# Kernel tuning notes

Measured on AMD Instinct MI355X. Metric: run time of the kernel, lower is better.

Reference implementation:

```python
import jax, jax.numpy as jnp
import numpy as np

B, C, H, W = 4, 256, 64, 64
N = H * W


def _conv1x1(x, w, b):
    # x: [B,C,H,W], w: [O,C], b: [O]  (1x1 conv == per-pixel linear)
    return jnp.einsum('bchw,oc->bohw', x, w) + b[None, :, None, None]


def setup_inputs() -> dict:
    key = jax.random.key(0)
    ks = jax.random.split(key, 11)
    s = 1.0 / np.sqrt(C)
    x = jax.random.normal(ks[0], (B, C, H, W), dtype=jnp.float32)
    mkw = lambda k: jax.random.normal(k, (C, C), dtype=jnp.float32) * s
    mkb = lambda k: jax.random.normal(k, (C,), dtype=jnp.float32) * 0.01
    return {
        'x': x,
        'w_teta': mkw(ks[1]), 'b_teta': mkb(ks[2]),
        'w_fi': mkw(ks[3]), 'b_fi': mkb(ks[4]),
        'w_gi': mkw(ks[5]), 'b_gi': mkb(ks[6]),
        'w_o1': mkw(ks[7]), 'b_o1': mkb(ks[8]),
        'w_o2': mkw(ks[9]), 'b_o2': mkb(ks[10]),
    }


def reference(x, w_teta, b_teta, w_fi, b_fi, w_gi, b_gi, w_o1, b_o1, w_o2, b_o2):
    b, c, h, w = x.shape
    n = h * w
    # 1x1 projections, flattened to [B,C,N]
    x1 = _conv1x1(x, w_teta, b_teta).reshape(b, c, n)
    x2 = _conv1x1(x, w_fi, b_fi).reshape(b, c, n)
    x3 = _conv1x1(x, w_gi, b_gi).reshape(b, c, n)
    # NOTE: original uses .view (memory reinterpretation), NOT transpose
    x1 = x1.reshape(b, n, c)
    x3 = x3.reshape(b, n, c)
    scores = jnp.einsum('bnc,bcm->bnm', x1, x2)      # [B,N,N]
    s_row = jax.nn.softmax(scores, axis=2)
    s_col = jax.nn.softmax(scores, axis=1)
    y1 = jnp.einsum('bnm,bmc->bnc', s_row, x3)       # [B,N,C]
    y2 = jnp.einsum('bnm,bmc->bnc', s_col, x3)
    # transpose(1,2) then view -> contiguous transpose + reshape
    y1 = jnp.swapaxes(y1, 1, 2).reshape(b, c, h, w)
    y2 = jnp.swapaxes(y2, 1, 2).reshape(b, c, h, w)
    o1 = _conv1x1(y1, w_o1, b_o1)
    o2 = _conv1x1(y2, w_o2, b_o2)
    xx = jnp.concatenate([x, x], axis=1)             # [B,2C,H,W]
    agg = jnp.concatenate([o1, o2], axis=1)
    return jax.nn.relu(xx + agg)
```

## Files before the change

kernel.cpp:

```cpp
#include <hip/hip_runtime.h>

#define BB   4
#define CC   256
#define NPIX 4096
#define AST2 40
#define YST  72

typedef __attribute__((ext_vector_type(8)))  short bf16x8;
typedef __attribute__((ext_vector_type(8)))  _Float16 f16x8;
typedef __attribute__((ext_vector_type(4)))  short short4v;
typedef __attribute__((ext_vector_type(16))) float f32x16;

__device__ __forceinline__ short f2h(float f) {
    _Float16 h = (_Float16)f;
    return __builtin_bit_cast(short, h);
}
__device__ __forceinline__ int cdrow(int r, int l5) {
    return (r & 3) + 8 * (r >> 2) + 4 * l5;
}
__device__ __forceinline__ short s_enc(float v) {
    float c = fmaxf(fminf(v, 127.9f), -127.9f);
    return (short)__float2int_rn(c * 256.0f);
}
__device__ __forceinline__ float s_dec(short v) {
    return (float)v * (1.0f / 256.0f);
}

__device__ __forceinline__ void mfma_core_f16(
    const short* __restrict__ A, const short* __restrict__ B, f32x16 acc[2][2])
{
    __shared__ short LA[128 * AST2], LB[128 * AST2];
    const int t = threadIdx.x;
    const int lane = t & 63, w = t >> 6;
    const int l31 = lane & 31, l5 = lane >> 5;
    const int nq = (w & 1) * 64, mq = (w >> 1) * 64;
    const int sr = t >> 1;
    const int sk = (t & 1) * 16;
    const size_t gs = (size_t)sr * 256 + sk;
    const int ls = sr * AST2 + sk;

    bf16x8 rA0 = *(const bf16x8*)(A + gs);
    bf16x8 rA1 = *(const bf16x8*)(A + gs + 8);
    bf16x8 rB0 = *(const bf16x8*)(B + gs);
    bf16x8 rB1 = *(const bf16x8*)(B + gs + 8);

    for (int k0 = 0; k0 < 256; k0 += 32) {
        __syncthreads();
        *(bf16x8*)&LA[ls]     = rA0;
        *(bf16x8*)&LA[ls + 8] = rA1;
        *(bf16x8*)&LB[ls]     = rB0;
        *(bf16x8*)&LB[ls + 8] = rB1;
        __syncthreads();
        if (k0 + 32 < 256) {
            size_t g = gs + k0 + 32;
            rA0 = *(const bf16x8*)(A + g);
            rA1 = *(const bf16x8*)(A + g + 8);
            rB0 = *(const bf16x8*)(B + g);
            rB1 = *(const bf16x8*)(B + g + 8);
        }
#pragma unroll
        for (int ks = 0; ks < 2; ks++) {
            f16x8 a[2], b[2];
#pragma unroll
            for (int s = 0; s < 2; s++) {
                a[s] = *(const f16x8*)&LA[(nq + s * 32 + l31) * AST2 + ks * 16 + l5 * 8];
                b[s] = *(const f16x8*)&LB[(mq + s * 32 + l31) * AST2 + ks * 16 + l5 * 8];
            }
#pragma unroll
            for (int s = 0; s < 2; s++)
#pragma unroll
                for (int u = 0; u < 2; u++)
                    acc[s][u] = __builtin_amdgcn_mfma_f32_32x32x16_f16(a[s], b[u], acc[s][u], 0, 0, 0);
        }
    }
}


__global__ __launch_bounds__(256) void pack_w5(
    const float* __restrict__ w0, const float* __restrict__ w1,
    const float* __restrict__ w2, const float* __restrict__ w3,
    const float* __restrict__ w4, short* __restrict__ wall)
{
    int which = blockIdx.y;
    const float* w = which == 0 ? w0 : which == 1 ? w1 : which == 2 ? w2
                   : which == 3 ? w3 : w4;
    int idx = blockIdx.x * 1024 + threadIdx.x * 4;
    float4 v = *(const float4*)(w + idx);
    short4v h;
    h.x = f2h(v.x); h.y = f2h(v.y); h.z = f2h(v.z); h.w = f2h(v.w);
    *(short4v*)(wall + which * 65536 + idx) = h;
}

__global__ __launch_bounds__(256) void pack_t_f16(
    const float* __restrict__ in, short* __restrict__ o16)
{
    __shared__ short T[32][36];
    const int b  = blockIdx.z;
    const int n0 = blockIdx.x * 32;
    const int c0 = blockIdx.y * 32;
    const float* src = in + (size_t)b * CC * NPIX;
    const int t = threadIdx.x;
    const int r = t >> 3, q = t & 7;
    float4 v = *(const float4*)(src + (size_t)(c0 + r) * NPIX + n0 + q * 4);
    T[q * 4 + 0][r] = f2h(v.x);
    T[q * 4 + 1][r] = f2h(v.y);
    T[q * 4 + 2][r] = f2h(v.z);
    T[q * 4 + 3][r] = f2h(v.w);
    __syncthreads();
    short4v o;
    o.x = T[r][q * 4 + 0];
    o.y = T[r][q * 4 + 1];
    o.z = T[r][q * 4 + 2];
    o.w = T[r][q * 4 + 3];
    size_t oo = (size_t)b * CC * NPIX + (size_t)(n0 + r) * 256 + c0 + q * 4;
    *(short4v*)(o16 + oo) = o;
}

__global__ __launch_bounds__(256) void tr16_cn(
    const short* __restrict__ in, short* __restrict__ outp)
{
    __shared__ short T[32][33];
    const int b  = blockIdx.z;
    const int n0 = blockIdx.x * 32;
    const int c0 = blockIdx.y * 32;
    const short* src = in + (size_t)b * CC * NPIX;
    short* dst = outp + (size_t)b * CC * NPIX;
    const int t = threadIdx.x;
    const int r = t >> 3, q = t & 7;
    short4v v = *(const short4v*)(src + (size_t)(c0 + r) * NPIX + n0 + q * 4);
    T[q * 4 + 0][r] = v.x;
    T[q * 4 + 1][r] = v.y;
    T[q * 4 + 2][r] = v.z;
    T[q * 4 + 3][r] = v.w;
    __syncthreads();
    short4v o;
    o.x = T[r][q * 4 + 0];
    o.y = T[r][q * 4 + 1];
    o.z = T[r][q * 4 + 2];
    o.w = T[r][q * 4 + 3];
    *(short4v*)(dst + (size_t)(n0 + r) * 256 + c0 + q * 4) = o;
}

__global__ __launch_bounds__(256) void packVt_bf(
    const short* __restrict__ x3f, short* __restrict__ Vt)
{
    __shared__ short T[32][33];
    const int b  = blockIdx.z;
    const int m0 = blockIdx.x * 32;
    const int c0 = blockIdx.y * 32;
    const short* in = x3f + (size_t)b * CC * NPIX;
    short* out = Vt + (size_t)b * CC * NPIX;
    const int t = threadIdx.x;
    const int r = t >> 3, q = t & 7;
    short4v v = *(const short4v*)(in + (size_t)(m0 + r) * CC + c0 + q * 4);
    T[q * 4 + 0][r] = v.x;
    T[q * 4 + 1][r] = v.y;
    T[q * 4 + 2][r] = v.z;
    T[q * 4 + 3][r] = v.w;
    __syncthreads();
    short4v o;
    o.x = T[r][q * 4 + 0];
    o.y = T[r][q * 4 + 1];
    o.z = T[r][q * 4 + 2];
    o.w = T[r][q * 4 + 3];
    *(short4v*)(out + (size_t)(c0 + r) * NPIX + m0 + q * 4) = o;
}


__global__ __launch_bounds__(256) void proj_mfma(
    const short* __restrict__ wpf, const short* __restrict__ xtf,
    const float* __restrict__ b_teta, const float* __restrict__ b_fi,
    const float* __restrict__ b_gi,
    short* __restrict__ x1f, short* __restrict__ x2f, short* __restrict__ x3f)
{
    const int z = blockIdx.z, p = z >> 2, b = z & 3;
    const int n0 = blockIdx.x * 128, c0 = blockIdx.y * 128;
    const size_t CN = (size_t)CC * NPIX;
    const short* Ah = wpf + p * 65536 + c0 * 256;
    const short* Bh = xtf + (size_t)b * CN + (size_t)n0 * 256;
    const float* bias = p == 0 ? b_teta : p == 1 ? b_fi : b_gi;
    short* dst = p == 0 ? x1f : p == 1 ? x2f : x3f;

    f32x16 acc[2][2] = {};
    mfma_core_f16(Ah, Bh, acc);

    const int t = threadIdx.x, lane = t & 63, w = t >> 6;
    const int l31 = lane & 31, l5 = lane >> 5;
    const int aq = (w & 1) * 64, bq = (w >> 1) * 64;
#pragma unroll
    for (int s = 0; s < 2; s++)
#pragma unroll
        for (int u = 0; u < 2; u++)
#pragma unroll
            for (int r = 0; r < 16; r++) {
                int c = c0 + aq + s * 32 + cdrow(r, l5);
                int n = n0 + bq + u * 32 + l31;
                float v = acc[s][u][r] + bias[c];
                size_t o = (size_t)b * CN + (size_t)c * NPIX + n;
                dst[o] = f2h(v);
            }
}

__global__ __launch_bounds__(256) void scores_mfma(
    const short* __restrict__ x1f, const short* __restrict__ x2tf,
    short* __restrict__ S16, float* __restrict__ pm, float* __restrict__ pl)
{
    const int m0 = blockIdx.x * 128, n0 = blockIdx.y * 128;
    f32x16 acc[2][2] = {};
    mfma_core_f16(x1f + (size_t)n0 * 256, x2tf + (size_t)m0 * 256, acc);

    const int t = threadIdx.x, lane = t & 63, w = t >> 6;
    const int l31 = lane & 31, l5 = lane >> 5;
    const int aq = (w & 1) * 64, bq = (w >> 1) * 64;
#pragma unroll
    for (int s = 0; s < 2; s++)
#pragma unroll
        for (int u = 0; u < 2; u++)
#pragma unroll
            for (int r = 0; r < 16; r++) {
                int n = n0 + aq + s * 32 + cdrow(r, l5);
                int m = m0 + bq + u * 32 + l31;
                S16[(size_t)n * NPIX + m] = s_enc(acc[s][u][r]);
            }

    const int member = w & 1;
#pragma unroll
    for (int u = 0; u < 2; u++) {
        float vmax = -1e30f;
#pragma unroll
        for (int s = 0; s < 2; s++)
#pragma unroll
            for (int r = 0; r < 16; r++) vmax = fmaxf(vmax, acc[s][u][r]);
        float vsum = 0.0f;
#pragma unroll
        for (int s = 0; s < 2; s++)
#pragma unroll
            for (int r = 0; r < 16; r++) vsum += __expf(acc[s][u][r] - vmax);
        float vmax2 = __shfl_xor(vmax, 32, 64);
        float vsum2 = __shfl_xor(vsum, 32, 64);
        float mc = fmaxf(vmax, vmax2);
        float sc = vsum * __expf(vmax - mc) + vsum2 * __expf(vmax2 - mc);
        if (l5 == 0) {
            size_t pidx = (size_t)(blockIdx.y * 2 + member) * NPIX + m0 + bq + u * 32 + l31;
            pm[pidx] = mc;
            pl[pidx] = sc;
        }
    }
}

__global__ __launch_bounds__(256) void out_mfma(
    const short* __restrict__ wof,
    const float* __restrict__ b_o1, const float* __restrict__ b_o2,
    const short* __restrict__ Yp,
    const float* __restrict__ x, float* __restrict__ out, int b)
{
    __shared__ short LA[128 * AST2], LB[128 * AST2];
    const size_t CN_ = (size_t)NPIX * CC;
    const int ch0 = blockIdx.y * 128;
    const int pix0 = blockIdx.x * 128;
    const int mode = ch0 < 256 ? 0 : 1;
    const short* W = wof + mode * 65536 + (size_t)(ch0 & 255) * 256;
    const short* Yq = Yp + (size_t)mode * 4 * CN_;
    const float* bias = mode == 0 ? b_o1 : b_o2;

    const int t = threadIdx.x, lane = t & 63, w = t >> 6;
    const int l31 = lane & 31, l5 = lane >> 5;
    const int nq = (w & 1) * 64, mq = (w >> 1) * 64;
    const int sr = t >> 1;
    const int sk = (t & 1) * 16;
    const size_t gsA = (size_t)sr * 256 + sk;
    const size_t gsB = (size_t)(pix0 + sr) * 256 + sk;
    const int ls = sr * AST2 + sk;

    f32x16 acc[2][2] = {};

    bf16x8 rA0 = *(const bf16x8*)(W + gsA);
    bf16x8 rA1 = *(const bf16x8*)(W + gsA + 8);
    f16x8 rB0, rB1;
    {
        f16x8 a0 = *(const f16x8*)(Yq + gsB);
        f16x8 a1 = *(const f16x8*)(Yq + CN_ + gsB);
        f16x8 a2 = *(const f16x8*)(Yq + 2 * CN_ + gsB);
        f16x8 a3 = *(const f16x8*)(Yq + 3 * CN_ + gsB);
        rB0 = (a0 + a1) + (a2 + a3);
        f16x8 c0 = *(const f16x8*)(Yq + gsB + 8);
        f16x8 c1 = *(const f16x8*)(Yq + CN_ + gsB + 8);
        f16x8 c2 = *(const f16x8*)(Yq + 2 * CN_ + gsB + 8);
        f16x8 c3 = *(const f16x8*)(Yq + 3 * CN_ + gsB + 8);
        rB1 = (c0 + c1) + (c2 + c3);
    }

    for (int k0 = 0; k0 < 256; k0 += 32) {
        __syncthreads();
        *(bf16x8*)&LA[ls]    = rA0;
        *(bf16x8*)&LA[ls + 8] = rA1;
        *(f16x8*)&LB[ls]     = rB0;
        *(f16x8*)&LB[ls + 8] = rB1;
        __syncthreads();
        if (k0 + 32 < 256) {
            size_t gA = gsA + k0 + 32;
            size_t gB = gsB + k0 + 32;
            rA0 = *(const bf16x8*)(W + gA);
            rA1 = *(const bf16x8*)(W + gA + 8);
            f16x8 a0 = *(const f16x8*)(Yq + gB);
            f16x8 a1 = *(const f16x8*)(Yq + CN_ + gB);
            f16x8 a2 = *(const f16x8*)(Yq + 2 * CN_ + gB);
            f16x8 a3 = *(const f16x8*)(Yq + 3 * CN_ + gB);
            rB0 = (a0 + a1) + (a2 + a3);
            f16x8 c0 = *(const f16x8*)(Yq + gB + 8);
            f16x8 c1 = *(const f16x8*)(Yq + CN_ + gB + 8);
            f16x8 c2 = *(const f16x8*)(Yq + 2 * CN_ + gB + 8);
            f16x8 c3 = *(const f16x8*)(Yq + 3 * CN_ + gB + 8);
            rB1 = (c0 + c1) + (c2 + c3);
        }
#pragma unroll
        for (int ks = 0; ks < 2; ks++) {
            f16x8 a[2], bb[2];
#pragma unroll
            for (int s = 0; s < 2; s++) {
                a[s]  = *(const f16x8*)&LA[(nq + s * 32 + l31) * AST2 + ks * 16 + l5 * 8];
                bb[s] = *(const f16x8*)&LB[(mq + s * 32 + l31) * AST2 + ks * 16 + l5 * 8];
            }
#pragma unroll
            for (int s = 0; s < 2; s++)
#pragma unroll
                for (int u = 0; u < 2; u++)
                    acc[s][u] = __builtin_amdgcn_mfma_f32_32x32x16_f16(a[s], bb[u], acc[s][u], 0, 0, 0);
        }
    }

    const int aq = (w & 1) * 64, bq = (w >> 1) * 64;
#pragma unroll
    for (int s = 0; s < 2; s++)
#pragma unroll
        for (int u = 0; u < 2; u++)
#pragma unroll
            for (int r = 0; r < 16; r++) {
                int ch = ch0 + aq + s * 32 + cdrow(r, l5);
                int pix = pix0 + bq + u * 32 + l31;
                int chm = ch & 255;
                float v = acc[s][u][r] + bias[chm] +
                          x[((size_t)b * CC + chm) * NPIX + pix];
                out[((size_t)b * 2 * CC + ch) * NPIX + pix] = fmaxf(v, 0.0f);
            }
}

__global__ __launch_bounds__(256) void colstats2_kernel(
    const float* __restrict__ pm, const float* __restrict__ pl,
    float* __restrict__ cm, float* __restrict__ cli)
{
    __shared__ float sm[4][64], sl[4][64];
    const int t = threadIdx.x;
    const int cl = t & 63, ch = t >> 6;
    const int col = blockIdx.x * 64 + cl;
    float m = -1e30f, l = 0.0f;
    for (int i = ch * 16; i < ch * 16 + 16; i++) {
        float m2 = pm[(size_t)i * NPIX + col];
        float l2 = pl[(size_t)i * NPIX + col];
        float mn = fmaxf(m, m2);
        l = l * __expf(m - mn) + l2 * __expf(m2 - mn);
        m = mn;
    }
    sm[ch][cl] = m;
    sl[ch][cl] = l;
    __syncthreads();
    if (ch == 0) {
#pragma unroll
        for (int j = 1; j < 4; j++) {
            float m2 = sm[j][cl], l2 = sl[j][cl];
            float mn = fmaxf(m, m2);
            l = l * __expf(m - mn) + l2 * __expf(m2 - mn);
            m = mn;
        }
        cm[col]  = m;
        cli[col] = 1.0f / l;
    }
}

__global__ __launch_bounds__(256) void rowexpP_kernel(
    const short* __restrict__ S16,
    const float* __restrict__ colm, const float* __restrict__ colli,
    short* __restrict__ P1, short* __restrict__ P2)
{
    const int row = blockIdx.x;
    const short* sp = S16 + (size_t)row * NPIX;
    const int t = threadIdx.x;
    const int w = t >> 6, lane = t & 63;
    __shared__ float red[4];

    float s4[16];
#pragma unroll
    for (int i = 0; i < 4; i++) {
        short4v v = *(const short4v*)(sp + (i * 256 + t) * 4);
        s4[i * 4 + 0] = s_dec(v.x);
        s4[i * 4 + 1] = s_dec(v.y);
        s4[i * 4 + 2] = s_dec(v.z);
        s4[i * 4 + 3] = s_dec(v.w);
    }

    float m = -1e30f;
#pragma unroll
    for (int i = 0; i < 16; i++) m = fmaxf(m, s4[i]);
    for (int off = 32; off; off >>= 1) m = fmaxf(m, __shfl_xor(m, off, 64));
    if (lane == 0) red[w] = m;
    __syncthreads();
    m = fmaxf(fmaxf(red[0], red[1]), fmaxf(red[2], red[3]));
    __syncthreads();

    float e[16];
    float sum = 0.0f;
#pragma unroll
    for (int i = 0; i < 16; i++) {
        e[i] = __expf(s4[i] - m);
        sum += e[i];
    }
    for (int off = 32; off; off >>= 1) sum += __shfl_xor(sum, off, 64);
    if (lane == 0) red[w] = sum;
    __syncthreads();
    float rl = 1.0f / (red[0] + red[1] + red[2] + red[3]);

    short* p1 = P1 + (size_t)row * NPIX;
    short* p2 = P2 + (size_t)row * NPIX;
#pragma unroll
    for (int i = 0; i < 4; i++) {
        int idx = (i * 256 + t) * 4;
        float4 cm4 = *(const float4*)(colm + idx);
        float4 cl4 = *(const float4*)(colli + idx);
        short4v a, bvv;
        a.x = f2h(e[i * 4 + 0] * rl);
        a.y = f2h(e[i * 4 + 1] * rl);
        a.z = f2h(e[i * 4 + 2] * rl);
        a.w = f2h(e[i * 4 + 3] * rl);
        bvv.x = f2h(__expf(s4[i * 4 + 0] - cm4.x) * cl4.x);
        bvv.y = f2h(__expf(s4[i * 4 + 1] - cm4.y) * cl4.y);
        bvv.z = f2h(__expf(s4[i * 4 + 2] - cm4.z) * cl4.z);
        bvv.w = f2h(__expf(s4[i * 4 + 3] - cm4.w) * cl4.w);
        *(short4v*)(p1 + idx) = a;
        *(short4v*)(p2 + idx) = bvv;
    }
}

__global__ __launch_bounds__(256) void ygemm_kernel(
    const short* __restrict__ P1, const short* __restrict__ P2,
    const short* __restrict__ Vt, short* __restrict__ Yp)
{
    __shared__ short LA[64 * YST];
    __shared__ short LB[256 * YST];
    const int mode = blockIdx.z, kq = blockIdx.y;
    const int n0 = blockIdx.x * 64;
    const short* A = (mode ? P2 : P1) + (size_t)n0 * NPIX;
    const short* B = Vt;
    const int kbase = kq * 1024;

    const int t = threadIdx.x, lane = t & 63, w = t >> 6;
    const int l31 = lane & 31, l5 = lane >> 5;
    const int nst = (w & 1) * 32, cb = (w >> 1) * 128;
    const int ar = t >> 2;
    const int ak = (t & 3) * 16;

    bf16x8 pa[2], pb[8];
    {
        const short* ap = A + (size_t)ar * NPIX + kbase + ak;
        pa[0] = *(const bf16x8*)ap;
        pa[1] = *(const bf16x8*)(ap + 8);
#pragma unroll
        for (int i = 0; i < 4; i++) {
            const short* bp = B + (size_t)(i * 64 + ar) * NPIX + kbase + ak;
            pb[2 * i]     = *(const bf16x8*)bp;
            pb[2 * i + 1] = *(const bf16x8*)(bp + 8);
        }
    }

    f32x16 acc[4] = {};
    for (int s = 0; s < 16; s++) {
        __syncthreads();
        *(bf16x8*)&LA[ar * YST + ak]     = pa[0];
        *(bf16x8*)&LA[ar * YST + ak + 8] = pa[1];
#pragma unroll
        for (int i = 0; i < 4; i++) {
            *(bf16x8*)&LB[(i * 64 + ar) * YST + ak]     = pb[2 * i];
            *(bf16x8*)&LB[(i * 64 + ar) * YST + ak + 8] = pb[2 * i + 1];
        }
        __syncthreads();
        if (s + 1 < 16) {
            int kg = kbase + (s + 1) * 64 + ak;
            const short* ap = A + (size_t)ar * NPIX + kg;
            pa[0] = *(const bf16x8*)ap;
            pa[1] = *(const bf16x8*)(ap + 8);
#pragma unroll
            for (int i = 0; i < 4; i++) {
                const short* bp = B + (size_t)(i * 64 + ar) * NPIX + kg;
                pb[2 * i]     = *(const bf16x8*)bp;
                pb[2 * i + 1] = *(const bf16x8*)(bp + 8);
            }
        }
#pragma unroll
        for (int kc = 0; kc < 4; kc++) {
            f16x8 af = *(const f16x8*)&LA[(nst + l31) * YST + kc * 16 + l5 * 8];
#pragma unroll
            for (int u = 0; u < 4; u++) {
                f16x8 bf = *(const f16x8*)&LB[(cb + u * 32 + l31) * YST + kc * 16 + l5 * 8];
                acc[u] = __builtin_amdgcn_mfma_f32_32x32x16_f16(af, bf, acc[u], 0, 0, 0);
            }
        }
    }

    short* Yo = Yp + (size_t)(mode * 4 + kq) * ((size_t)NPIX * CC);
#pragma unroll
    for (int u = 0; u < 4; u++)
#pragma unroll
        for (int r = 0; r < 16; r++) {
            int rr = cdrow(r, l5);
            Yo[(size_t)(n0 + nst + rr) * CC + cb + u * 32 + l31] = f2h(acc[u][r]);
        }
}

extern "C" void kernel_launch(void* const* d_in, const int* in_sizes, int n_in,
                              void* d_out, int out_size, void* d_ws, size_t ws_size,
                              hipStream_t stream)
{
    (void)in_sizes; (void)n_in; (void)out_size; (void)ws_size;
    const float* x      = (const float*)d_in[0];
    const float* w_teta = (const float*)d_in[1];
    const float* b_teta = (const float*)d_in[2];
    const float* w_fi   = (const float*)d_in[3];
    const float* b_fi   = (const float*)d_in[4];
    const float* w_gi   = (const float*)d_in[5];
    const float* b_gi   = (const float*)d_in[6];
    const float* w_o1   = (const float*)d_in[7];
    const float* b_o1   = (const float*)d_in[8];
    const float* w_o2   = (const float*)d_in[9];
    const float* b_o2   = (const float*)d_in[10];
    float* out = (float*)d_out;

    const size_t CN = (size_t)CC * NPIX;
    const size_t NN = (size_t)NPIX * NPIX;
    short* wsp   = (short*)d_ws;
    short* S16   = wsp;
    short* P1    = S16 + NN;
    short* P2    = P1 + NN;
    short* Yp    = P2 + NN;
    short* x1f   = Yp + 8 * CN;
    short* x2tf  = x1f + BB * CN;
    short* Vtb   = x2tf + BB * CN;
    float* cm    = (float*)(Vtb + BB * CN);
    float* cli   = cm + NPIX;
    float* pm    = cli + NPIX;
    float* pl    = pm + 64 * NPIX;
    short* wall  = (short*)(pl + 64 * NPIX);
    short* wpf   = wall;
    short* wof   = wall + 3 * 65536;
    short* xtf  = P1;
    short* x2f  = P2;
    short* x3f  = x2f + BB * CN;

    dim3 blk(256);
    pack_w5<<<dim3(64, 5), blk, 0, stream>>>(w_teta, w_fi, w_gi, w_o1, w_o2, wall);
    pack_t_f16<<<dim3(128, 8, 4), blk, 0, stream>>>(x, xtf);

    proj_mfma<<<dim3(32, 2, 12), blk, 0, stream>>>(
        wpf, xtf, b_teta, b_fi, b_gi, x1f, x2f, x3f);

    tr16_cn<<<dim3(128, 8, 4), blk, 0, stream>>>(x2f, x2tf);
    packVt_bf<<<dim3(128, 8, 4), blk, 0, stream>>>(x3f, Vtb);

    for (int b = 0; b < BB; b++) {
        scores_mfma<<<dim3(32, 32), blk, 0, stream>>>(
            x1f + b * CN, x2tf + b * CN, S16, pm, pl);
        colstats2_kernel<<<dim3(64), blk, 0, stream>>>(pm, pl, cm, cli);
        rowexpP_kernel<<<dim3(4096), blk, 0, stream>>>(S16, cm, cli, P1, P2);
        ygemm_kernel<<<dim3(64, 4, 2), blk, 0, stream>>>(
            P1, P2, Vtb + b * CN, Yp);
        out_mfma<<<dim3(32, 4), blk, 0, stream>>>(
            wof, b_o1, b_o2, Yp, x, out, b);
    }
}
```

Measured before the change: 473.3 us.

## Fuse softmax probability generation into PV GEMM, computing row/col stats only

The separate pass that wrote the full P1 and P2 half-precision probability matrices is removed. A stats kernel now computes column stats together with per-row max and inverse sum in a single launch. The PV GEMM reads the quantized scores directly and forms the exponentials on the fly for either the row or the column softmax. This drops two N×N writes and reads per batch in exchange for recomputing exp in the GEMM loop, with the S16 tile read by both modes and four kq blocks.

After: 455.8 us. 1.04x faster.

```diff
diff --git a/kernel.cpp b/kernel.cpp
--- a/kernel.cpp
+++ b/kernel.cpp
@@ -345,111 +345,84 @@
             }
 }
 
-__global__ __launch_bounds__(256) void colstats2_kernel(
+__global__ __launch_bounds__(256) void stats16_kernel(
+    const short* __restrict__ S16,
     const float* __restrict__ pm, const float* __restrict__ pl,
-    float* __restrict__ cm, float* __restrict__ cli)
+    float* __restrict__ cm, float* __restrict__ cli,
+    float* __restrict__ rm, float* __restrict__ rli)
 {
     __shared__ float sm[4][64], sl[4][64];
+    __shared__ float red[4];
     const int t = threadIdx.x;
-    const int cl = t & 63, ch = t >> 6;
-    const int col = blockIdx.x * 64 + cl;
-    float m = -1e30f, l = 0.0f;
-    for (int i = ch * 16; i < ch * 16 + 16; i++) {
-        float m2 = pm[(size_t)i * NPIX + col];
-        float l2 = pl[(size_t)i * NPIX + col];
-        float mn = fmaxf(m, m2);
-        l = l * __expf(m - mn) + l2 * __expf(m2 - mn);
-        m = mn;
-    }
-    sm[ch][cl] = m;
-    sl[ch][cl] = l;
-    __syncthreads();
-    if (ch == 0) {
-#pragma unroll
-        for (int j = 1; j < 4; j++) {
-            float m2 = sm[j][cl], l2 = sl[j][cl];
+    if (blockIdx.x < 64) {
+        const int cl = t & 63, ch = t >> 6;
+        const int col = blockIdx.x * 64 + cl;
+        float m = -1e30f, l = 0.0f;
+        for (int i = ch * 16; i < ch * 16 + 16; i++) {
+            float m2 = pm[(size_t)i * NPIX + col];
+            float l2 = pl[(size_t)i * NPIX + col];
             float mn = fmaxf(m, m2);
             l = l * __expf(m - mn) + l2 * __expf(m2 - mn);
             m = mn;
         }
-        cm[col]  = m;
-        cli[col] = 1.0f / l;
-    }
-}
-
-__global__ __launch_bounds__(256) void rowexpP_kernel(
-    const short* __restrict__ S16,
-    const float* __restrict__ colm, const float* __restrict__ colli,
-    short* __restrict__ P1, short* __restrict__ P2)
-{
-    const int row = blockIdx.x;
-    const short* sp = S16 + (size_t)row * NPIX;
-    const int t = threadIdx.x;
-    const int w = t >> 6, lane = t & 63;
-    __shared__ float red[4];
-
-    float s4[16];
-#pragma unroll
-    for (int i = 0; i < 4; i++) {
-        short4v v = *(const short4v*)(sp + (i * 256 + t) * 4);
-        s4[i * 4 + 0] = s_dec(v.x);
-        s4[i * 4 + 1] = s_dec(v.y);
-        s4[i * 4 + 2] = s_dec(v.z);
-        s4[i * 4 + 3] = s_dec(v.w);
-    }
-
-    float m = -1e30f;
-#pragma unroll
-    for (int i = 0; i < 16; i++) m = fmaxf(m, s4[i]);
-    for (int off = 32; off; off >>= 1) m = fmaxf(m, __shfl_xor(m, off, 64));
-    if (lane == 0) red[w] = m;
-    __syncthreads();
-    m = fmaxf(fmaxf(red[0], red[1]), fmaxf(red[2], red[3]));
-    __syncthreads();
-
-    float e[16];
-    float sum = 0.0f;
-#pragma unroll
-    for (int i = 0; i < 16; i++) {
-        e[i] = __expf(s4[i] - m);
-        sum += e[i];
-    }
-    for (int off = 32; off; off >>= 1) sum += __shfl_xor(sum, off, 64);
-    if (lane == 0) red[w] = sum;
-    __syncthreads();
-    float rl = 1.0f / (red[0] + red[1] + red[2] + red[3]);
-
-    short* p1 = P1 + (size_t)row * NPIX;
-    short* p2 = P2 + (size_t)row * NPIX;
-#pragma unroll
-    for (int i = 0; i < 4; i++) {
-        int idx = (i * 256 + t) * 4;
-        float4 cm4 = *(const float4*)(colm + idx);
-        float4 cl4 = *(const float4*)(colli + idx);
-        short4v a, bvv;
-        a.x = f2h(e[i * 4 + 0] * rl);
-        a.y = f2h(e[i * 4 + 1] * rl);
-        a.z = f2h(e[i * 4 + 2] * rl);
-        a.w = f2h(e[i * 4 + 3] * rl);
-        bvv.x = f2h(__expf(s4[i * 4 + 0] - cm4.x) * cl4.x);
-        bvv.y = f2h(__expf(s4[i * 4 + 1] - cm4.y) * cl4.y);
-        bvv.z = f2h(__expf(s4[i * 4 + 2] - cm4.z) * cl4.z);
-        bvv.w = f2h(__expf(s4[i * 4 + 3] - cm4.w) * cl4.w);
-        *(short4v*)(p1 + idx) = a;
-        *(short4v*)(p2 + idx) = bvv;
-    }
-}
-
-__global__ __launch_bounds__(256) void ygemm_kernel(
-    const short* __restrict__ P1, const short* __restrict__ P2,
-    const short* __restrict__ Vt, short* __restrict__ Yp)
+        sm[ch][cl] = m;
+        sl[ch][cl] = l;
+        __syncthreads();
+        if (ch == 0) {
+#pragma unroll
+            for (int j = 1; j < 4; j++) {
+                float m2 = sm[j][cl], l2 = sl[j][cl];
+                float mn = fmaxf(m, m2);
+                l = l * __expf(m - mn) + l2 * __expf(m2 - mn);
+                m = mn;
+            }
+            cm[col]  = m;
+            cli[col] = 1.0f / l;
+        }
+    } else {
+        const int row = blockIdx.x - 64;
+        const short* sp = S16 + (size_t)row * NPIX;
+        const int w = t >> 6, lane = t & 63;
+        float s4[16];
+#pragma unroll
+        for (int i = 0; i < 4; i++) {
+            short4v v = *(const short4v*)(sp + (i * 256 + t) * 4);
+            s4[i * 4 + 0] = s_dec(v.x);
+            s4[i * 4 + 1] = s_dec(v.y);
+            s4[i * 4 + 2] = s_dec(v.z);
+            s4[i * 4 + 3] = s_dec(v.w);
+        }
+        float m = -1e30f;
+#pragma unroll
+        for (int i = 0; i < 16; i++) m = fmaxf(m, s4[i]);
+        for (int off = 32; off; off >>= 1) m = fmaxf(m, __shfl_xor(m, off, 64));
+        if (lane == 0) red[w] = m;
+        __syncthreads();
+        m = fmaxf(fmaxf(red[0], red[1]), fmaxf(red[2], red[3]));
+        __syncthreads();
+        float sum = 0.0f;
+#pragma unroll
+        for (int i = 0; i < 16; i++) sum += __expf(s4[i] - m);
+        for (int off = 32; off; off >>= 1) sum += __shfl_xor(sum, off, 64);
+        if (lane == 0) red[w] = sum;
+        __syncthreads();
+        if (t == 0) {
+            rm[row]  = m;
+            rli[row] = 1.0f / (red[0] + red[1] + red[2] + red[3]);
+        }
+    }
+}
+
+__global__ __launch_bounds__(256) void pv_kernel(
+    const short* __restrict__ S16, const short* __restrict__ Vt,
+    const float* __restrict__ rmv, const float* __restrict__ rliv,
+    const float* __restrict__ cmv, const float* __restrict__ cliv,
+    short* __restrict__ Yp)
 {
     __shared__ short LA[64 * YST];
     __shared__ short LB[256 * YST];
     const int mode = blockIdx.z, kq = blockIdx.y;
     const int n0 = blockIdx.x * 64;
-    const short* A = (mode ? P2 : P1) + (size_t)n0 * NPIX;
-    const short* B = Vt;
     const int kbase = kq * 1024;
 
     const int t = threadIdx.x, lane = t & 63, w = t >> 6;
@@ -458,24 +431,49 @@
     const int ar = t >> 2;
     const int ak = (t & 3) * 16;
 
-    bf16x8 pa[2], pb[8];
-    {
-        const short* ap = A + (size_t)ar * NPIX + kbase + ak;
-        pa[0] = *(const bf16x8*)ap;
-        pa[1] = *(const bf16x8*)(ap + 8);
-#pragma unroll
-        for (int i = 0; i < 4; i++) {
-            const short* bp = B + (size_t)(i * 64 + ar) * NPIX + kbase + ak;
-            pb[2 * i]     = *(const bf16x8*)bp;
-            pb[2 * i + 1] = *(const bf16x8*)(bp + 8);
-        }
+    const float mrow = rmv[n0 + ar];
+    const float lrow = rliv[n0 + ar];
+    const short* sp = S16 + (size_t)(n0 + ar) * NPIX + kbase + ak;
+
+    short4v sv[4];
+    bf16x8 pb[8];
+#pragma unroll
+    for (int i = 0; i < 4; i++)
+        sv[i] = *(const short4v*)(sp + i * 4);
+#pragma unroll
+    for (int i = 0; i < 4; i++) {
+        const short* bp = Vt + (size_t)(i * 64 + ar) * NPIX + kbase + ak;
+        pb[2 * i]     = *(const bf16x8*)bp;
+        pb[2 * i + 1] = *(const bf16x8*)(bp + 8);
     }
 
     f32x16 acc[4] = {};
     for (int s = 0; s < 16; s++) {
-        __syncthreads();
-        *(bf16x8*)&LA[ar * YST + ak]     = pa[0];
-        *(bf16x8*)&LA[ar * YST + ak + 8] = pa[1];
+        short4v ph[4];
+        if (mode == 0) {
+#pragma unroll
+            for (int i = 0; i < 4; i++) {
+                ph[i].x = f2h(__expf(s_dec(sv[i].x) - mrow) * lrow);
+                ph[i].y = f2h(__expf(s_dec(sv[i].y) - mrow) * lrow);
+                ph[i].z = f2h(__expf(s_dec(sv[i].z) - mrow) * lrow);
+                ph[i].w = f2h(__expf(s_dec(sv[i].w) - mrow) * lrow);
+            }
+        } else {
+            const int mg = kbase + s * 64 + ak;
+#pragma unroll
+            for (int i = 0; i < 4; i++) {
+                float4 cm4 = *(const float4*)(cmv + mg + i * 4);
+                float4 cl4 = *(const float4*)(cliv + mg + i * 4);
+                ph[i].x = f2h(__expf(s_dec(sv[i].x) - cm4.x) * cl4.x);
+                ph[i].y = f2h(__expf(s_dec(sv[i].y) - cm4.y) * cl4.y);
+                ph[i].z = f2h(__expf(s_dec(sv[i].z) - cm4.z) * cl4.z);
+                ph[i].w = f2h(__expf(s_dec(sv[i].w) - cm4.w) * cl4.w);
+            }
+        }
+        __syncthreads();
+#pragma unroll
+        for (int i = 0; i < 4; i++)
+            *(short4v*)&LA[ar * YST + ak + i * 4] = ph[i];
 #pragma unroll
         for (int i = 0; i < 4; i++) {
             *(bf16x8*)&LB[(i * 64 + ar) * YST + ak]     = pb[2 * i];
@@ -483,13 +481,14 @@
         }
         __syncthreads();
         if (s + 1 < 16) {
+            const short* spn = sp + (s + 1) * 64;
+#pragma unroll
+            for (int i = 0; i < 4; i++)
+                sv[i] = *(const short4v*)(spn + i * 4);
             int kg = kbase + (s + 1) * 64 + ak;
-            const short* ap = A + (size_t)ar * NPIX + kg;
-            pa[0] = *(const bf16x8*)ap;
-            pa[1] = *(const bf16x8*)(ap + 8);
 #pragma unroll
             for (int i = 0; i < 4; i++) {
-                const short* bp = B + (size_t)(i * 64 + ar) * NPIX + kg;
+                const short* bp = Vt + (size_t)(i * 64 + ar) * NPIX + kg;
                 pb[2 * i]     = *(const bf16x8*)bp;
                 pb[2 * i + 1] = *(const bf16x8*)(bp + 8);
             }
@@ -537,22 +536,22 @@
     const size_t NN = (size_t)NPIX * NPIX;
     short* wsp   = (short*)d_ws;
     short* S16   = wsp;
-    short* P1    = S16 + NN;
-    short* P2    = P1 + NN;
-    short* Yp    = P2 + NN;
+    short* Yp    = S16 + NN;
     short* x1f   = Yp + 8 * CN;
     short* x2tf  = x1f + BB * CN;
     short* Vtb   = x2tf + BB * CN;
     float* cm    = (float*)(Vtb + BB * CN);
     float* cli   = cm + NPIX;
-    float* pm    = cli + NPIX;
+    float* rm    = cli + NPIX;
+    float* rli   = rm + NPIX;
+    float* pm    = rli + NPIX;
     float* pl    = pm + 64 * NPIX;
     short* wall  = (short*)(pl + 64 * NPIX);
     short* wpf   = wall;
     short* wof   = wall + 3 * 65536;
-    short* xtf  = P1;
-    short* x2f  = P2;
-    short* x3f  = x2f + BB * CN;
+    short* xtf  = Yp;
+    short* x2f  = S16;
+    short* x3f  = S16 + BB * CN;
 
     dim3 blk(256);
     pack_w5<<<dim3(64, 5), blk, 0, stream>>>(w_teta, w_fi, w_gi, w_o1, w_o2, wall);
@@ -567,10 +566,10 @@
     for (int b = 0; b < BB; b++) {
         scores_mfma<<<dim3(32, 32), blk, 0, stream>>>(
             x1f + b * CN, x2tf + b * CN, S16, pm, pl);
-        colstats2_kernel<<<dim3(64), blk, 0, stream>>>(pm, pl, cm, cli);
-        rowexpP_kernel<<<dim3(4096), blk, 0, stream>>>(S16, cm, cli, P1, P2);
-        ygemm_kernel<<<dim3(64, 4, 2), blk, 0, stream>>>(
-            P1, P2, Vtb + b * CN, Yp);
+        stats16_kernel<<<dim3(64 + NPIX), blk, 0, stream>>>(
+            S16, pm, pl, cm, cli, rm, rli);
+        pv_kernel<<<dim3(64, 4, 2), blk, 0, stream>>>(
+            S16, Vtb + b * CN, rm, rli, cm, cli, Yp);
         out_mfma<<<dim3(32, 4), blk, 0, stream>>>(
             wof, b_o1, b_o2, Yp, x, out, b);
     }
```
